# Performance work log

Measured on AMD Instinct MI355X. Metric: run time of the kernel, lower is better.

The kernel has to match this reference:

```python
import jax, jax.numpy as jnp
import numpy as np

TOK, IN, OUT = 4096, 4096, 12288


def setup_inputs() -> dict:
    key = jax.random.key(0)
    k1, k2, k3, k4 = jax.random.split(key, 4)
    x = jax.random.normal(k1, (TOK, IN), dtype=jnp.float32)
    # int8 weight stored [out, in] (module transposes to this layout)
    weight = jax.random.randint(k2, (OUT, IN), -128, 128, dtype=jnp.int32).astype(jnp.int8)
    # per-output-channel dequant scale (positive, realistic magnitude)
    weight_scale = jax.random.uniform(k3, (OUT,), dtype=jnp.float32) * 0.02 + 1e-3
    bias = jax.random.normal(k4, (OUT,), dtype=jnp.float32) * 0.01
    return {"x": x, "weight": weight, "weight_scale": weight_scale, "bias": bias}


def reference(x, weight, weight_scale, bias):
    # --- dynamic per-token activation quantization ---
    amax = jnp.max(jnp.abs(x), axis=-1, keepdims=True)          # [TOK, 1]
    act_scale = jnp.maximum(amax / 127.0, 1e-8)                  # per-token scale
    x_q = jnp.clip(jnp.round(x / act_scale), -128, 127).astype(jnp.int8)
    # --- int8 GEMM accumulating in int32: y = x_q @ W^T ---
    acc = jax.lax.dot_general(
        x_q, weight,
        dimension_numbers=(((1,), (1,)), ((), ())),
        preferred_element_type=jnp.int32,
    )                                                            # [TOK, OUT] int32
    # --- dequant: per-token act scale * per-channel weight scale, + bias ---
    return acc.astype(jnp.float32) * act_scale * weight_scale + bias
```

## Files before the change

kernel.cpp:

```cpp
#include <hip/hip_runtime.h>
#include <stdint.h>

#define TOK  4096
#define KIN  4096
#define NOUT 12288

#define BM 128
#define BN 128
#define BK 64

typedef __attribute__((ext_vector_type(4))) int int32x4;

__global__ __launch_bounds__(256) void repack_w(const int* __restrict__ w32,
                                                int8_t* __restrict__ w8)
{
    const size_t i = (size_t)blockIdx.x * 256 + threadIdx.x;
    const int4 v = ((const int4*)w32)[i];
    unsigned pack = ((unsigned)(uint8_t)(int8_t)v.x)
                  | ((unsigned)(uint8_t)(int8_t)v.y << 8)
                  | ((unsigned)(uint8_t)(int8_t)v.z << 16)
                  | ((unsigned)(uint8_t)(int8_t)v.w << 24);
    ((int*)w8)[i] = (int)pack;
}

__global__ __launch_bounds__(256) void quant_rows(const float* __restrict__ x,
                                                  int8_t* __restrict__ xq,
                                                  float* __restrict__ ascale)
{
    const int row = blockIdx.x;
    const int tid = threadIdx.x;
    const float4* xr = (const float4*)(x + (size_t)row * KIN);

    float4 v[4];
    float m = 0.0f;
#pragma unroll
    for (int i = 0; i < 4; ++i) {
        v[i] = xr[tid + 256 * i];
        m = fmaxf(m, fmaxf(fmaxf(fabsf(v[i].x), fabsf(v[i].y)),
                           fmaxf(fabsf(v[i].z), fabsf(v[i].w))));
    }
#pragma unroll
    for (int off = 32; off > 0; off >>= 1)
        m = fmaxf(m, __shfl_down(m, off, 64));
    __shared__ float wm[4];
    if ((tid & 63) == 0) wm[tid >> 6] = m;
    __syncthreads();
    const float amax = fmaxf(fmaxf(wm[0], wm[1]), fmaxf(wm[2], wm[3]));
    const float s   = fmaxf(amax / 127.0f, 1e-8f);
    const float inv = 1.0f / s;
    if (tid == 0) ascale[row] = s;

    int* out32 = (int*)(xq + (size_t)row * KIN);
#pragma unroll
    for (int i = 0; i < 4; ++i) {
        float c[4] = {v[i].x, v[i].y, v[i].z, v[i].w};
        unsigned pack = 0;
#pragma unroll
        for (int j = 0; j < 4; ++j) {
            float r = rintf(c[j] * inv);
            r = fminf(fmaxf(r, -128.0f), 127.0f);
            pack |= ((unsigned)(uint8_t)(int8_t)(int)r) << (8 * j);
        }
        out32[tid + 256 * i] = (int)pack;
    }
}

#define GLOAD_LDS16(g, l)                                                     \
    __builtin_amdgcn_global_load_lds(                                         \
        (const __attribute__((address_space(1))) unsigned int*)(g),           \
        (__attribute__((address_space(3))) unsigned int*)(l), 16, 0, 0)

__global__ __launch_bounds__(256) void gemm_i8(const int8_t* __restrict__ A,
                                               const int8_t* __restrict__ B,
                                               const float* __restrict__ ascale,
                                               const float* __restrict__ wscale,
                                               const float* __restrict__ bias,
                                               float* __restrict__ C)
{
    __shared__ __align__(16) int8_t As[BM * BK];
    __shared__ __align__(16) int8_t Bs[BN * BK];

    const int tid  = threadIdx.x;
    const int lane = tid & 63;
    const int wave = tid >> 6;
    const int quad = lane >> 4;
    const int l16  = lane & 15;
    const int wm   = (wave >> 1) * 64;
    const int wn   = (wave & 1) * 64;
    const int m0   = blockIdx.y * BM;
    const int n0   = blockIdx.x * BN;

    int32x4 acc[4][4];
#pragma unroll
    for (int i = 0; i < 4; ++i)
#pragma unroll
        for (int j = 0; j < 4; ++j) acc[i][j] = (int32x4){0, 0, 0, 0};

    const int p0 = tid, p1 = tid + 256;
    const int r0 = p0 >> 2, ch0 = ((p0 & 3) - (r0 >> 1)) & 3;
    const int r1 = p1 >> 2, ch1 = ((p1 & 3) - (r1 >> 1)) & 3;
    const int8_t* gA0 = A + (size_t)(m0 + r0) * KIN + ch0 * 16;
    const int8_t* gA1 = A + (size_t)(m0 + r1) * KIN + ch1 * 16;
    const int8_t* gB0 = B + (size_t)(n0 + r0) * KIN + ch0 * 16;
    const int8_t* gB1 = B + (size_t)(n0 + r1) * KIN + ch1 * 16;
    int8_t* lA0 = As + p0 * 16;
    int8_t* lA1 = As + p1 * 16;
    int8_t* lB0 = Bs + p0 * 16;
    int8_t* lB1 = Bs + p1 * 16;

    for (int kk = 0; kk < KIN; kk += BK) {
        __syncthreads();
        GLOAD_LDS16(gA0 + kk, lA0);
        GLOAD_LDS16(gA1 + kk, lA1);
        GLOAD_LDS16(gB0 + kk, lB0);
        GLOAD_LDS16(gB1 + kk, lB1);
        __syncthreads();

        int32x4 aF[4], bF[4];
#pragma unroll
        for (int t = 0; t < 4; ++t) {
            const int rA = wm + t * 16 + l16;
            aF[t] = *(const int32x4*)(As + rA * 64 +
                                      ((quad + (rA >> 1)) & 3) * 16);
        }
#pragma unroll
        for (int t = 0; t < 4; ++t) {
            const int rB = wn + t * 16 + l16;
            bF[t] = *(const int32x4*)(Bs + rB * 64 +
                                      ((quad + (rB >> 1)) & 3) * 16);
        }

#pragma unroll
        for (int i = 0; i < 4; ++i)
#pragma unroll
            for (int j = 0; j < 4; ++j)
                acc[i][j] = __builtin_amdgcn_mfma_i32_16x16x64_i8(
                    aF[i], bF[j], acc[i][j], 0, 0, 0);
    }

#pragma unroll
    for (int i = 0; i < 4; ++i) {
        const int mb = m0 + wm + i * 16 + quad * 4;
        const float as0 = ascale[mb + 0];
        const float as1 = ascale[mb + 1];
        const float as2 = ascale[mb + 2];
        const float as3 = ascale[mb + 3];
#pragma unroll
        for (int j = 0; j < 4; ++j) {
            const int n   = n0 + wn + j * 16 + l16;
            const float wsn = wscale[n];
            const float bn  = bias[n];
            float* Cp = C + (size_t)mb * NOUT + n;
            Cp[0 * (size_t)NOUT] = (float)acc[i][j][0] * as0 * wsn + bn;
            Cp[1 * (size_t)NOUT] = (float)acc[i][j][1] * as1 * wsn + bn;
            Cp[2 * (size_t)NOUT] = (float)acc[i][j][2] * as2 * wsn + bn;
            Cp[3 * (size_t)NOUT] = (float)acc[i][j][3] * as3 * wsn + bn;
        }
    }
}

extern "C" void kernel_launch(void* const* d_in, const int* in_sizes, int n_in,
                              void* d_out, int out_size, void* d_ws, size_t ws_size,
                              hipStream_t stream)
{
    (void)in_sizes; (void)n_in; (void)out_size; (void)ws_size;
    const float* x      = (const float*)d_in[0];
    const int*   w32    = (const int*)d_in[1];
    const float* wscale = (const float*)d_in[2];
    const float* bias   = (const float*)d_in[3];
    float*       out    = (float*)d_out;

    int8_t* xq     = (int8_t*)d_ws;
    float*  ascale = (float*)((char*)d_ws + (size_t)TOK * KIN);
    int8_t* w8     = (int8_t*)((char*)d_ws + (size_t)TOK * KIN + 65536);

    repack_w<<<(size_t)NOUT * KIN / 4 / 256, 256, 0, stream>>>(w32, w8);
    quant_rows<<<TOK, 256, 0, stream>>>(x, xq, ascale);
    dim3 grid(NOUT / BN, TOK / BM);
    gemm_i8<<<grid, 256, 0, stream>>>(xq, w8, ascale, wscale, bias, out);
}
```

Measured before the change: 610.8 us.

## Rewrite int8 GEMM as 256x256 double-buffered pipelined kernel with XOR swizzle

Replaces the 128x128 single-buffered GEMM with a 256x256 tile using 512 threads, BK=128, and double-buffered LDS. Global-to-LDS loads for later k-steps are interleaved with MFMA phases, controlled by manual waitcnt, barriers and setprio. It also adds an XOR LDS swizzle and a workgroup remap for L2 locality. The aim is to hide load latency and raise arithmetic intensity, at the cost of much more LDS and register use per block, which may lower occupancy.

```diff
diff --git a/kernel.cpp b/kernel.cpp
--- a/kernel.cpp
+++ b/kernel.cpp
@@ -5,9 +5,10 @@
 #define KIN  4096
 #define NOUT 12288
 
-#define BM 128
-#define BN 128
-#define BK 64
+#define BM  256
+#define BN  256
+#define BKB 128
+#define NKT (KIN / BKB)
 
 typedef __attribute__((ext_vector_type(4))) int int32x4;
 
@@ -70,91 +71,133 @@
         (const __attribute__((address_space(1))) unsigned int*)(g),           \
         (__attribute__((address_space(3))) unsigned int*)(l), 16, 0, 0)
 
-__global__ __launch_bounds__(256) void gemm_i8(const int8_t* __restrict__ A,
-                                               const int8_t* __restrict__ B,
-                                               const float* __restrict__ ascale,
-                                               const float* __restrict__ wscale,
-                                               const float* __restrict__ bias,
-                                               float* __restrict__ C)
-{
-    __shared__ __align__(16) int8_t As[BM * BK];
-    __shared__ __align__(16) int8_t Bs[BN * BK];
-
-    const int tid  = threadIdx.x;
+#define STAGE_A(bufb, R0, kk)                                                 \
+    GLOAD_LDS16(gA + (size_t)(R0) * KIN + (kk),                               \
+                lA + (bufb) * 32768 + (R0) * 128)
+#define STAGE_B(bufb, s, R0, kk)                                              \
+    GLOAD_LDS16(gB + (size_t)(R0) * KIN + (kk) + (s) * 64,                    \
+                lB + (bufb) * 32768 + (s) * 16384 + (R0) * 64)
+
+#define PHASE(cur, mh, ks, STAGES, TAILWAIT)                                  \
+    {                                                                         \
+        const int abase = (cur) * 32768 + (mh) * 8192 + ((ks) ? aA1 : aA0);   \
+        const int bbase = (cur) * 32768 + (ks) * 16384 + bA;                  \
+        int32x4 af[4], bf[4];                                                 \
+        _Pragma("unroll")                                                     \
+        for (int u = 0; u < 4; ++u)                                           \
+            af[u] = *(const int32x4*)(As + abase + u * 2048);                 \
+        _Pragma("unroll")                                                     \
+        for (int u = 0; u < 4; ++u)                                           \
+            bf[u] = *(const int32x4*)(Bs + bbase + u * 1024);                 \
+        STAGES;                                                               \
+        __builtin_amdgcn_s_barrier();                                         \
+        asm volatile("s_waitcnt lgkmcnt(0)" ::: "memory");                    \
+        __builtin_amdgcn_sched_barrier(0);                                    \
+        __builtin_amdgcn_s_setprio(1);                                        \
+        _Pragma("unroll")                                                     \
+        for (int fi = 0; fi < 4; ++fi)                                        \
+            _Pragma("unroll")                                                 \
+            for (int fj = 0; fj < 4; ++fj)                                    \
+                acc[(mh) * 4 + fi][fj] =                                      \
+                    __builtin_amdgcn_mfma_i32_16x16x64_i8(                    \
+                        af[fi], bf[fj], acc[(mh) * 4 + fi][fj], 0, 0, 0);     \
+        __builtin_amdgcn_s_setprio(0);                                        \
+        TAILWAIT;                                                             \
+        __builtin_amdgcn_s_barrier();                                         \
+        asm volatile("" ::: "memory");                                        \
+    }
+
+__global__ __launch_bounds__(512, 2) void gemm_i8(const int8_t* __restrict__ A,
+                                                  const int8_t* __restrict__ B,
+                                                  const float* __restrict__ ascale,
+                                                  const float* __restrict__ wscale,
+                                                  const float* __restrict__ bias,
+                                                  float* __restrict__ C)
+{
+    __shared__ __align__(16) int8_t As[2 * BM * BKB];
+    __shared__ __align__(16) int8_t Bs[2 * 2 * BN * 64];
+
+    const int tid  = (int)threadIdx.x;
     const int lane = tid & 63;
     const int wave = tid >> 6;
     const int quad = lane >> 4;
     const int l16  = lane & 15;
-    const int wm   = (wave >> 1) * 64;
-    const int wn   = (wave & 1) * 64;
-    const int m0   = blockIdx.y * BM;
-    const int n0   = blockIdx.x * BN;
-
-    int32x4 acc[4][4];
-#pragma unroll
-    for (int i = 0; i < 4; ++i)
+    const int wr   = wave >> 2;
+    const int wc   = wave & 3;
+
+    const int nbx  = NOUT / BN;
+    const int wgid = (int)blockIdx.x;
+    const int swz  = (wgid & 7) * (((TOK / BM) * nbx) >> 3) + (wgid >> 3);
+    const int bx   = swz % nbx;
+    const int by   = swz / nbx;
+    const int m0   = by * BM;
+    const int n0   = bx * BN;
+
+    int32x4 acc[8][4];
+#pragma unroll
+    for (int i = 0; i < 8; ++i)
 #pragma unroll
         for (int j = 0; j < 4; ++j) acc[i][j] = (int32x4){0, 0, 0, 0};
 
-    const int p0 = tid, p1 = tid + 256;
-    const int r0 = p0 >> 2, ch0 = ((p0 & 3) - (r0 >> 1)) & 3;
-    const int r1 = p1 >> 2, ch1 = ((p1 & 3) - (r1 >> 1)) & 3;
-    const int8_t* gA0 = A + (size_t)(m0 + r0) * KIN + ch0 * 16;
-    const int8_t* gA1 = A + (size_t)(m0 + r1) * KIN + ch1 * 16;
-    const int8_t* gB0 = B + (size_t)(n0 + r0) * KIN + ch0 * 16;
-    const int8_t* gB1 = B + (size_t)(n0 + r1) * KIN + ch1 * 16;
-    int8_t* lA0 = As + p0 * 16;
-    int8_t* lA1 = As + p1 * 16;
-    int8_t* lB0 = Bs + p0 * 16;
-    int8_t* lB1 = Bs + p1 * 16;
-
-    for (int kk = 0; kk < KIN; kk += BK) {
-        __syncthreads();
-        GLOAD_LDS16(gA0 + kk, lA0);
-        GLOAD_LDS16(gA1 + kk, lA1);
-        GLOAD_LDS16(gB0 + kk, lB0);
-        GLOAD_LDS16(gB1 + kk, lB1);
-        __syncthreads();
-
-        int32x4 aF[4], bF[4];
-#pragma unroll
-        for (int t = 0; t < 4; ++t) {
-            const int rA = wm + t * 16 + l16;
-            aF[t] = *(const int32x4*)(As + rA * 64 +
-                                      ((quad + (rA >> 1)) & 3) * 16);
-        }
-#pragma unroll
-        for (int t = 0; t < 4; ++t) {
-            const int rB = wn + t * 16 + l16;
-            bF[t] = *(const int32x4*)(Bs + rB * 64 +
-                                      ((quad + (rB >> 1)) & 3) * 16);
-        }
-
-#pragma unroll
-        for (int i = 0; i < 4; ++i)
-#pragma unroll
-            for (int j = 0; j < 4; ++j)
-                acc[i][j] = __builtin_amdgcn_mfma_i32_16x16x64_i8(
-                    aF[i], bF[j], acc[i][j], 0, 0, 0);
-    }
-
-#pragma unroll
-    for (int i = 0; i < 4; ++i) {
-        const int mb = m0 + wm + i * 16 + quad * 4;
+    const int arow = tid >> 3;
+    const int8_t* gA = A + (size_t)(m0 + arow) * KIN
+                         + (((tid & 7) ^ (arow & 7)) << 4);
+    const int brow = tid >> 2;
+    const int8_t* gB = B + (size_t)(n0 + brow) * KIN
+                         + ((((tid & 3) ^ ((tid >> 3) & 3))) << 4);
+    int8_t* lA = As + tid * 16;
+    int8_t* lB = Bs + tid * 16;
+
+    const int aA0 = (wr * 128 + l16) * 128 + (((0 + quad) ^ (l16 & 7)) << 4);
+    const int aA1 = (wr * 128 + l16) * 128 + (((4 + quad) ^ (l16 & 7)) << 4);
+    const int bA  = (wc * 64 + l16) * 64 + ((quad ^ ((l16 >> 1) & 3)) << 4);
+
+    STAGE_A(0, 0, 0);      STAGE_A(0, 128, 0);
+    STAGE_A(0, 64, 0);     STAGE_A(0, 192, 0);
+    STAGE_B(0, 0, 0, 0);   STAGE_B(0, 0, 128, 0);
+    STAGE_B(0, 1, 0, 0);   STAGE_B(0, 1, 128, 0);
+    STAGE_B(1, 0, 0, BKB); STAGE_B(1, 0, 128, BKB);
+    STAGE_A(1, 64, BKB);   STAGE_A(1, 192, BKB);
+    asm volatile("s_waitcnt vmcnt(4)" ::: "memory");
+    __builtin_amdgcn_s_barrier();
+    asm volatile("" ::: "memory");
+
+#pragma unroll 1
+    for (int g = 0; g < NKT; g += 2) {
+        const int k1 = (g + 1) * BKB;
+        const int k2 = (g + 2 < NKT ? g + 2 : NKT - 1) * BKB;
+        const int k3 = (g + 3 < NKT ? g + 3 : NKT - 1) * BKB;
+        PHASE(0, 0, 0, { STAGE_A(1, 0, k1);    STAGE_A(1, 128, k1);
+                         STAGE_B(1, 1, 0, k1); STAGE_B(1, 1, 128, k1); }, )
+        PHASE(0, 1, 0, , )
+        PHASE(0, 1, 1, { STAGE_B(0, 0, 0, k2); STAGE_B(0, 0, 128, k2); }, )
+        PHASE(0, 0, 1, { STAGE_A(0, 64, k2);   STAGE_A(0, 192, k2); },
+              asm volatile("s_waitcnt vmcnt(4)" ::: "memory"))
+        PHASE(1, 0, 0, { STAGE_A(0, 0, k2);    STAGE_A(0, 128, k2);
+                         STAGE_B(0, 1, 0, k2); STAGE_B(0, 1, 128, k2); }, )
+        PHASE(1, 1, 0, , )
+        PHASE(1, 1, 1, { STAGE_B(1, 0, 0, k3); STAGE_B(1, 0, 128, k3); }, )
+        PHASE(1, 0, 1, { STAGE_A(1, 64, k3);   STAGE_A(1, 192, k3); },
+              asm volatile("s_waitcnt vmcnt(4)" ::: "memory"))
+    }
+
+#pragma unroll
+    for (int fi = 0; fi < 8; ++fi) {
+        const int mb = m0 + wr * 128 + fi * 16 + quad * 4;
         const float as0 = ascale[mb + 0];
         const float as1 = ascale[mb + 1];
         const float as2 = ascale[mb + 2];
         const float as3 = ascale[mb + 3];
 #pragma unroll
-        for (int j = 0; j < 4; ++j) {
-            const int n   = n0 + wn + j * 16 + l16;
+        for (int fj = 0; fj < 4; ++fj) {
+            const int n = n0 + wc * 64 + fj * 16 + l16;
             const float wsn = wscale[n];
             const float bn  = bias[n];
             float* Cp = C + (size_t)mb * NOUT + n;
-            Cp[0 * (size_t)NOUT] = (float)acc[i][j][0] * as0 * wsn + bn;
-            Cp[1 * (size_t)NOUT] = (float)acc[i][j][1] * as1 * wsn + bn;
-            Cp[2 * (size_t)NOUT] = (float)acc[i][j][2] * as2 * wsn + bn;
-            Cp[3 * (size_t)NOUT] = (float)acc[i][j][3] * as3 * wsn + bn;
+            Cp[0 * (size_t)NOUT] = (float)acc[fi][fj][0] * as0 * wsn + bn;
+            Cp[1 * (size_t)NOUT] = (float)acc[fi][fj][1] * as1 * wsn + bn;
+            Cp[2 * (size_t)NOUT] = (float)acc[fi][fj][2] * as2 * wsn + bn;
+            Cp[3 * (size_t)NOUT] = (float)acc[fi][fj][3] * as3 * wsn + bn;
         }
     }
 }
@@ -176,6 +219,6 @@
 
     repack_w<<<(size_t)NOUT * KIN / 4 / 256, 256, 0, stream>>>(w32, w8);
     quant_rows<<<TOK, 256, 0, stream>>>(x, xq, ascale);
-    dim3 grid(NOUT / BN, TOK / BM);
-    gemm_i8<<<grid, 256, 0, stream>>>(xq, w8, ascale, wscale, bias, out);
-}
+    gemm_i8<<<(TOK / BM) * (NOUT / BN), 512, 0, stream>>>(xq, w8, ascale,
+                                                          wscale, bias, out);
+}
```

Measured after the change: 570.9 us. 1.07x faster.
